# Optimization experiments

Measured on AMD Instinct MI355X. Metric: run time of the kernel, lower is better.

Reference implementation:

```python
import jax, jax.numpy as jnp
import numpy as np

N = 50000   # nodes
E = 800000  # edges (avg degree 16)
D = 128     # hidden_channels
L = 4       # num_layers
ALPHA = 0.1


def setup_inputs() -> dict:
    key = jax.random.key(0)
    ks = jax.random.split(key, 6)
    x = jax.random.normal(ks[0], (N, D), dtype=jnp.float32)
    w = jax.random.uniform(ks[1], (E,), dtype=jnp.float32)
    src = jax.random.randint(ks[2], (E,), 0, N)
    dst = jax.random.randint(ks[3], (E,), 0, N)
    # stacked per-layer Linear params
    W = jax.random.normal(ks[4], (L, D, D), dtype=jnp.float32) / np.float32(np.sqrt(D))
    b = jax.random.normal(ks[5], (L, D), dtype=jnp.float32) * 0.01
    # GPR coefficients: alpha*(1-alpha)^k, last = (1-alpha)^L
    temp_np = ALPHA * (1 - ALPHA) ** np.arange(L + 1)
    temp_np[-1] = (1 - ALPHA) ** L
    temp = jnp.asarray(temp_np, dtype=jnp.float32)
    return {"x": x, "w": w, "src": src, "dst": dst, "W": W, "b": b, "temp": temp}


def reference(x, w, src, dst, W, b, temp):
    # eval mode: dropout / dropout_adj are no-ops; edge_attn=False
    hidden = x * temp[0]
    for i in range(L):
        h = x @ W[i] + b[i]                 # [N, D] linear
        msg = h[src] * w[:, None]           # gather + edge-weight, [E, D]
        x = jax.ops.segment_sum(msg, dst, num_segments=N)  # scatter-sum
        x = jax.nn.relu(x)
        hidden = hidden + x * temp[i + 1]
    return hidden
```

## Files before the change

kernel.cpp:

```cpp
#include <hip/hip_runtime.h>
#include <hip/hip_fp16.h>

#define N_NODES 50000
#define N_EDGES 800000
#define DIM 128
#define LAYERS 4
#define SLOT 48
#define EPB 8

#define BUCKET_BLOCKS 3128
#define WT_BLOCKS 256
#define INIT_BLOCKS 6250

typedef __attribute__((ext_vector_type(8))) _Float16 half8;
typedef __attribute__((ext_vector_type(4))) float float4v;

__device__ __forceinline__ int pack_edge(int s, float w) {
    return (int)(((unsigned)__half_as_ushort(__float2half(w)) << 16) | (unsigned)(s & 0xFFFF));
}

__device__ __forceinline__ void bucket_one(int d, int s, float wv, int g,
                                           int* __restrict__ cnt,
                                           int* __restrict__ edge_buf) {
    if ((d & 7) == g) {
        int pos = atomicAdd(&cnt[d], 1);
        edge_buf[(size_t)d * SLOT + pos] = pack_edge(s, wv);
    }
}

__global__ __launch_bounds__(256) void prep_kernel(const int* __restrict__ src,
                                                   const int* __restrict__ dst,
                                                   const float* __restrict__ w,
                                                   int* __restrict__ cnt,
                                                   int* __restrict__ edge_buf,
                                                   const float* __restrict__ W,
                                                   __half* __restrict__ Wt,
                                                   const float4* __restrict__ x,
                                                   __half* __restrict__ xh) {
    int bid = blockIdx.x;
    int tid = threadIdx.x;
    if (bid < BUCKET_BLOCKS) {
        int g     = bid & 7;
        int chunk = bid >> 3;
        int base  = (chunk * 256 + tid) * EPB;
        if (base >= N_EDGES) return;
        int4   d4a = *(const int4*)(dst + base);
        int4   d4b = *(const int4*)(dst + base + 4);
        int4   s4a = *(const int4*)(src + base);
        int4   s4b = *(const int4*)(src + base + 4);
        float4 w4a = *(const float4*)(w + base);
        float4 w4b = *(const float4*)(w + base + 4);
        bucket_one(d4a.x, s4a.x, w4a.x, g, cnt, edge_buf);
        bucket_one(d4a.y, s4a.y, w4a.y, g, cnt, edge_buf);
        bucket_one(d4a.z, s4a.z, w4a.z, g, cnt, edge_buf);
        bucket_one(d4a.w, s4a.w, w4a.w, g, cnt, edge_buf);
        bucket_one(d4b.x, s4b.x, w4b.x, g, cnt, edge_buf);
        bucket_one(d4b.y, s4b.y, w4b.y, g, cnt, edge_buf);
        bucket_one(d4b.z, s4b.z, w4b.z, g, cnt, edge_buf);
        bucket_one(d4b.w, s4b.w, w4b.w, g, cnt, edge_buf);
    } else if (bid < BUCKET_BLOCKS + WT_BLOCKS) {
        int i = (bid - BUCKET_BLOCKS) * 256 + tid;
        int l   = i >> 14;
        int rem = i & 16383;
        int k = rem >> 7;
        int n = rem & 127;
        Wt[(size_t)l * DIM * DIM + n * DIM + k] =
            __float2half(W[(size_t)l * DIM * DIM + k * DIM + n]);
    } else {
        int i = (bid - BUCKET_BLOCKS - WT_BLOCKS) * 256 + tid;
        float4 v = x[i];
        union { __half2 hh[2]; float2 f2; } u;
        u.hh[0] = __floats2half2_rn(v.x, v.y);
        u.hh[1] = __floats2half2_rn(v.z, v.w);
        *(float2*)(xh + (size_t)i * 4) = u.f2;
    }
}

__device__ __forceinline__ void batch8(const half8* __restrict__ h8,
                                       int m, int base, int cnt_r, int r, int c,
                                       float* accf, float& wsum) {
    half8 v[8]; float wv[8];
    #pragma unroll
    for (int u = 0; u < 8; ++u) {
        int jj = base + u;
        int p  = __shfl(m, (r << 4) | (jj & 15), 64);
        bool live = (jj < cnt_r);
        wv[u] = live
                  ? __half2float(__ushort_as_half((unsigned short)((unsigned)p >> 16)))
                  : 0.f;
        half8 vv = (half8)(0.f);
        if (live) vv = h8[(size_t)(p & 0xFFFF) * 16 + c];
        v[u] = vv;
    }
    #pragma unroll
    for (int u = 0; u < 8; ++u) {
        wsum += wv[u];
        #pragma unroll
        for (int t = 0; t < 8; ++t)
            accf[t] += wv[u] * (float)v[u][t];
    }
}

#define AP 136
template <bool FINAL>
__global__ __launch_bounds__(256) void layer_kernel(const half8* __restrict__ xin8,
                                                    const int* __restrict__ cnt_arr,
                                                    const int* __restrict__ edge_buf,
                                                    const __half* __restrict__ Wt,
                                                    const float* __restrict__ bl,
                                                    __half* __restrict__ xout_h,
                                                    float* __restrict__ hidden,
                                                    const float* __restrict__ temp,
                                                    const float* __restrict__ xf,
                                                    const half8* __restrict__ x1h,
                                                    const half8* __restrict__ x2h) {
    __shared__ __half Ah[16][AP];
    __shared__ float winS[16];
    int tid  = threadIdx.x;
    int wave = tid >> 6;
    int lane = tid & 63;
    int r = lane >> 4;
    int c = lane & 15;
    int node0  = blockIdx.x * 16 + wave * 4;
    int node_r = node0 + r;

    size_t mb = (size_t)node_r * SLOT;
    int m0 = edge_buf[mb + c];
    int m1 = edge_buf[mb + 16 + c];
    int4 c4 = *(const int4*)(cnt_arr + node0);

    int cnt_r = (r == 0) ? c4.x : (r == 1) ? c4.y : (r == 2) ? c4.z : c4.w;
    int maxc  = max(max(c4.x, c4.y), max(c4.z, c4.w));

    float accf[8];
    #pragma unroll
    for (int t = 0; t < 8; ++t) accf[t] = 0.f;
    float wsum = 0.f;

    batch8(xin8, m0, 0, cnt_r, r, c, accf, wsum);
    batch8(xin8, m0, 8, cnt_r, r, c, accf, wsum);
    if (maxc > 16) {
        batch8(xin8, m1, 16, cnt_r, r, c, accf, wsum);
        batch8(xin8, m1, 24, cnt_r, r, c, accf, wsum);
    }
    if (maxc > 32) {
        int m2 = edge_buf[mb + 32 + c];
        batch8(xin8, m2, 32, cnt_r, r, c, accf, wsum);
        batch8(xin8, m2, 40, cnt_r, r, c, accf, wsum);
    }

    union { __half2 hh[4]; float4 f4; } ua;
    ua.hh[0] = __floats2half2_rn(accf[0], accf[1]);
    ua.hh[1] = __floats2half2_rn(accf[2], accf[3]);
    ua.hh[2] = __floats2half2_rn(accf[4], accf[5]);
    ua.hh[3] = __floats2half2_rn(accf[6], accf[7]);
    int lr = wave * 4 + r;
    *(float4*)&Ah[lr][c * 8] = ua.f4;
    if (c == 0) winS[lr] = wsum;
    __syncthreads();

    int am  = lane & 15;
    int ak8 = (lane >> 4) * 8;
    float4v acc0 = (float4v)(0.f), acc1 = (float4v)(0.f);
    #pragma unroll
    for (int kk = 0; kk < 4; ++kk) {
        int k0 = kk * 32 + ak8;
        half8 a  = *(const half8*)&Ah[am][k0];
        half8 b0 = *(const half8*)(Wt + (size_t)(wave * 32 + am) * DIM + k0);
        half8 b1 = *(const half8*)(Wt + (size_t)(wave * 32 + 16 + am) * DIM + k0);
        acc0 = __builtin_amdgcn_mfma_f32_16x16x32_f16(a, b0, acc0, 0, 0, 0);
        acc1 = __builtin_amdgcn_mfma_f32_16x16x32_f16(a, b1, acc1, 0, 0, 0);
    }
    __syncthreads();

    int q  = lane >> 4;
    int cc = lane & 15;
    {
        int col = wave * 32 + cc;
        float bv = bl[col];
        #pragma unroll
        for (int j = 0; j < 4; ++j) {
            int row = q * 4 + j;
            Ah[row][col] = __float2half(fmaxf(acc0[j] + winS[row] * bv, 0.f));
        }
        col = wave * 32 + 16 + cc;
        bv = bl[col];
        #pragma unroll
        for (int j = 0; j < 4; ++j) {
            int row = q * 4 + j;
            Ah[row][col] = __float2half(fmaxf(acc1[j] + winS[row] * bv, 0.f));
        }
    }
    __syncthreads();

    int row = tid >> 4;
    int ch  = tid & 15;
    int gnode = blockIdx.x * 16 + row;
    size_t o = (size_t)gnode * DIM + ch * 8;
    half8 hv = *(const half8*)&Ah[row][ch * 8];

    if constexpr (!FINAL) {
        *(float4*)(xout_h + o) = *(float4*)&hv;
    } else {
        float t0 = temp[0], t1 = temp[1], t2 = temp[2], t3 = temp[3], t4 = temp[4];
        size_t ro = (size_t)gnode * 16 + ch;
        half8 v1 = x1h[ro];
        half8 v2 = x2h[ro];
        half8 v3 = xin8[ro];
        float4 x0a = *(const float4*)(xf + o);
        float4 x0b = *(const float4*)(xf + o + 4);
        float out[8];
        out[0] = t0 * x0a.x; out[1] = t0 * x0a.y; out[2] = t0 * x0a.z; out[3] = t0 * x0a.w;
        out[4] = t0 * x0b.x; out[5] = t0 * x0b.y; out[6] = t0 * x0b.z; out[7] = t0 * x0b.w;
        #pragma unroll
        for (int t = 0; t < 8; ++t)
            out[t] += t1 * (float)v1[t] + t2 * (float)v2[t]
                    + t3 * (float)v3[t] + t4 * (float)hv[t];
        float4 h0 = make_float4(out[0], out[1], out[2], out[3]);
        float4 h1 = make_float4(out[4], out[5], out[6], out[7]);
        *(float4*)(hidden + o)     = h0;
        *(float4*)(hidden + o + 4) = h1;
    }
}

extern "C" void kernel_launch(void* const* d_in, const int* in_sizes, int n_in,
                              void* d_out, int out_size, void* d_ws, size_t ws_size,
                              hipStream_t stream) {
    const float* x    = (const float*)d_in[0];
    const float* w    = (const float*)d_in[1];
    const int*   src  = (const int*)d_in[2];
    const int*   dst  = (const int*)d_in[3];
    const float* W    = (const float*)d_in[4];
    const float* b    = (const float*)d_in[5];
    const float* temp = (const float*)d_in[6];
    float* hidden = (float*)d_out;

    char* ws = (char*)d_ws;
    __half* xhA      = (__half*)ws;                   ws += (size_t)N_NODES * DIM * sizeof(__half);
    __half* xhB      = (__half*)ws;                   ws += (size_t)N_NODES * DIM * sizeof(__half);
    __half* xhC      = (__half*)ws;                   ws += (size_t)N_NODES * DIM * sizeof(__half);
    __half* Wt       = (__half*)ws;                   ws += (size_t)LAYERS * DIM * DIM * sizeof(__half);
    int*    cnt      = (int*)ws;                      ws += (size_t)N_NODES * sizeof(int);
    int*    edge_buf = (int*)ws;                      ws += (size_t)(N_NODES * SLOT + 64) * sizeof(int);

    hipMemsetAsync(cnt, 0, (size_t)N_NODES * sizeof(int), stream);
    prep_kernel<<<BUCKET_BLOCKS + WT_BLOCKS + INIT_BLOCKS, 256, 0, stream>>>(
        src, dst, w, cnt, edge_buf, W, Wt, (const float4*)x, xhA);

    const int layer_blocks = N_NODES / 16;
    layer_kernel<false><<<layer_blocks, 256, 0, stream>>>(
        (const half8*)xhA, cnt, edge_buf, Wt + 0 * DIM * DIM, b + 0 * DIM,
        xhB, hidden, temp, x, nullptr, nullptr);
    layer_kernel<false><<<layer_blocks, 256, 0, stream>>>(
        (const half8*)xhB, cnt, edge_buf, Wt + 1 * DIM * DIM, b + 1 * DIM,
        xhC, hidden, temp, x, nullptr, nullptr);
    layer_kernel<false><<<layer_blocks, 256, 0, stream>>>(
        (const half8*)xhC, cnt, edge_buf, Wt + 2 * DIM * DIM, b + 2 * DIM,
        xhA, hidden, temp, x, nullptr, nullptr);
    layer_kernel<true><<<layer_blocks, 256, 0, stream>>>(
        (const half8*)xhA, cnt, edge_buf, Wt + 3 * DIM * DIM, b + 3 * DIM,
        nullptr, hidden, temp, x, (const half8*)xhB, (const half8*)xhC);
}
```

Measured before the change: 278.3 us.

## Store node features in FP8 and split edge packing from bucketing

Node feature buffers switch from fp16 to fp8 (e4m3 via the packed convert builtins), which halves the bytes moved by the per-edge gathers and the layer outputs. The final layer also reads x0 from the fp8 copy instead of the fp32 input. A separate pre-pass packs dst to 16 bits and src plus weight into one int, so the 8-way bucketing kernel rereads less data. FP8 storage adds noticeable quantization error, including on the x0 term, which may break the accuracy tolerance.

```diff
diff --git a/kernel.cpp b/kernel.cpp
--- a/kernel.cpp
+++ b/kernel.cpp
@@ -8,58 +8,64 @@
 #define SLOT 48
 #define EPB 8
 
+#define PACK_BLOCKS 782
+#define WT_BLOCKS 256
+#define INIT_BLOCKS 3125
 #define BUCKET_BLOCKS 3128
-#define WT_BLOCKS 256
-#define INIT_BLOCKS 6250
 
 typedef __attribute__((ext_vector_type(8))) _Float16 half8;
 typedef __attribute__((ext_vector_type(4))) float float4v;
+typedef __attribute__((ext_vector_type(2))) float float2v;
+typedef __attribute__((ext_vector_type(8))) unsigned short ushort8;
 
 __device__ __forceinline__ int pack_edge(int s, float w) {
     return (int)(((unsigned)__half_as_ushort(__float2half(w)) << 16) | (unsigned)(s & 0xFFFF));
 }
 
-__device__ __forceinline__ void bucket_one(int d, int s, float wv, int g,
-                                           int* __restrict__ cnt,
-                                           int* __restrict__ edge_buf) {
-    if ((d & 7) == g) {
-        int pos = atomicAdd(&cnt[d], 1);
-        edge_buf[(size_t)d * SLOT + pos] = pack_edge(s, wv);
-    }
-}
-
-__global__ __launch_bounds__(256) void prep_kernel(const int* __restrict__ src,
-                                                   const int* __restrict__ dst,
-                                                   const float* __restrict__ w,
-                                                   int* __restrict__ cnt,
-                                                   int* __restrict__ edge_buf,
-                                                   const float* __restrict__ W,
-                                                   __half* __restrict__ Wt,
-                                                   const float4* __restrict__ x,
-                                                   __half* __restrict__ xh) {
+__device__ __forceinline__ void fp8x8_to_f32(uint2 v, float* f) {
+    float2v a = __builtin_amdgcn_cvt_pk_f32_fp8(v.x, false);
+    float2v b = __builtin_amdgcn_cvt_pk_f32_fp8(v.x, true);
+    float2v c = __builtin_amdgcn_cvt_pk_f32_fp8(v.y, false);
+    float2v d = __builtin_amdgcn_cvt_pk_f32_fp8(v.y, true);
+    f[0] = a[0]; f[1] = a[1]; f[2] = b[0]; f[3] = b[1];
+    f[4] = c[0]; f[5] = c[1]; f[6] = d[0]; f[7] = d[1];
+}
+
+__device__ __forceinline__ uint2 f32x8_to_fp8(const float* f) {
+    unsigned lo = 0, hi = 0;
+    lo = __builtin_amdgcn_cvt_pk_fp8_f32(f[0], f[1], lo, false);
+    lo = __builtin_amdgcn_cvt_pk_fp8_f32(f[2], f[3], lo, true);
+    hi = __builtin_amdgcn_cvt_pk_fp8_f32(f[4], f[5], hi, false);
+    hi = __builtin_amdgcn_cvt_pk_fp8_f32(f[6], f[7], hi, true);
+    return make_uint2(lo, hi);
+}
+
+__global__ __launch_bounds__(256) void prep1_kernel(const int* __restrict__ src,
+                                                    const int* __restrict__ dst,
+                                                    const float* __restrict__ w,
+                                                    unsigned short* __restrict__ dst16,
+                                                    int* __restrict__ epk,
+                                                    const float* __restrict__ W,
+                                                    __half* __restrict__ Wt,
+                                                    const float4* __restrict__ x,
+                                                    uint2* __restrict__ xh0) {
     int bid = blockIdx.x;
     int tid = threadIdx.x;
-    if (bid < BUCKET_BLOCKS) {
-        int g     = bid & 7;
-        int chunk = bid >> 3;
-        int base  = (chunk * 256 + tid) * EPB;
-        if (base >= N_EDGES) return;
-        int4   d4a = *(const int4*)(dst + base);
-        int4   d4b = *(const int4*)(dst + base + 4);
-        int4   s4a = *(const int4*)(src + base);
-        int4   s4b = *(const int4*)(src + base + 4);
-        float4 w4a = *(const float4*)(w + base);
-        float4 w4b = *(const float4*)(w + base + 4);
-        bucket_one(d4a.x, s4a.x, w4a.x, g, cnt, edge_buf);
-        bucket_one(d4a.y, s4a.y, w4a.y, g, cnt, edge_buf);
-        bucket_one(d4a.z, s4a.z, w4a.z, g, cnt, edge_buf);
-        bucket_one(d4a.w, s4a.w, w4a.w, g, cnt, edge_buf);
-        bucket_one(d4b.x, s4b.x, w4b.x, g, cnt, edge_buf);
-        bucket_one(d4b.y, s4b.y, w4b.y, g, cnt, edge_buf);
-        bucket_one(d4b.z, s4b.z, w4b.z, g, cnt, edge_buf);
-        bucket_one(d4b.w, s4b.w, w4b.w, g, cnt, edge_buf);
-    } else if (bid < BUCKET_BLOCKS + WT_BLOCKS) {
-        int i = (bid - BUCKET_BLOCKS) * 256 + tid;
+    if (bid < PACK_BLOCKS) {
+        int e = (bid * 256 + tid) * 4;
+        if (e >= N_EDGES) return;
+        int4   d4 = *(const int4*)(dst + e);
+        int4   s4 = *(const int4*)(src + e);
+        float4 w4 = *(const float4*)(w + e);
+        uint2 dd;
+        dd.x = ((unsigned)d4.x & 0xFFFF) | ((unsigned)d4.y << 16);
+        dd.y = ((unsigned)d4.z & 0xFFFF) | ((unsigned)d4.w << 16);
+        *(uint2*)(dst16 + e) = dd;
+        int4 pk = make_int4(pack_edge(s4.x, w4.x), pack_edge(s4.y, w4.y),
+                            pack_edge(s4.z, w4.z), pack_edge(s4.w, w4.w));
+        *(int4*)(epk + e) = pk;
+    } else if (bid < PACK_BLOCKS + WT_BLOCKS) {
+        int i = (bid - PACK_BLOCKS) * 256 + tid;
         int l   = i >> 14;
         int rem = i & 16383;
         int k = rem >> 7;
@@ -67,19 +73,48 @@
         Wt[(size_t)l * DIM * DIM + n * DIM + k] =
             __float2half(W[(size_t)l * DIM * DIM + k * DIM + n]);
     } else {
-        int i = (bid - BUCKET_BLOCKS - WT_BLOCKS) * 256 + tid;
-        float4 v = x[i];
-        union { __half2 hh[2]; float2 f2; } u;
-        u.hh[0] = __floats2half2_rn(v.x, v.y);
-        u.hh[1] = __floats2half2_rn(v.z, v.w);
-        *(float2*)(xh + (size_t)i * 4) = u.f2;
-    }
-}
-
-__device__ __forceinline__ void batch8(const half8* __restrict__ h8,
+        int i = (bid - PACK_BLOCKS - WT_BLOCKS) * 256 + tid;
+        float4 a = x[(size_t)i * 2];
+        float4 b = x[(size_t)i * 2 + 1];
+        float f[8] = { a.x, a.y, a.z, a.w, b.x, b.y, b.z, b.w };
+        xh0[i] = f32x8_to_fp8(f);
+    }
+}
+
+__device__ __forceinline__ void bucket_one(int d, int pk, int g,
+                                           int* __restrict__ cnt,
+                                           int* __restrict__ edge_buf) {
+    if ((d & 7) == g) {
+        int pos = atomicAdd(&cnt[d], 1);
+        edge_buf[(size_t)d * SLOT + pos] = pk;
+    }
+}
+
+__global__ __launch_bounds__(256) void bucket_kernel(const unsigned short* __restrict__ dst16,
+                                                     const int* __restrict__ epk,
+                                                     int* __restrict__ cnt,
+                                                     int* __restrict__ edge_buf) {
+    int g     = blockIdx.x & 7;
+    int chunk = blockIdx.x >> 3;
+    int base  = (chunk * 256 + threadIdx.x) * EPB;
+    if (base >= N_EDGES) return;
+    ushort8 d8 = *(const ushort8*)(dst16 + base);
+    int4    pa = *(const int4*)(epk + base);
+    int4    pb = *(const int4*)(epk + base + 4);
+    bucket_one(d8[0], pa.x, g, cnt, edge_buf);
+    bucket_one(d8[1], pa.y, g, cnt, edge_buf);
+    bucket_one(d8[2], pa.z, g, cnt, edge_buf);
+    bucket_one(d8[3], pa.w, g, cnt, edge_buf);
+    bucket_one(d8[4], pb.x, g, cnt, edge_buf);
+    bucket_one(d8[5], pb.y, g, cnt, edge_buf);
+    bucket_one(d8[6], pb.z, g, cnt, edge_buf);
+    bucket_one(d8[7], pb.w, g, cnt, edge_buf);
+}
+
+__device__ __forceinline__ void batch8(const uint2* __restrict__ x8,
                                        int m, int base, int cnt_r, int r, int c,
                                        float* accf, float& wsum) {
-    half8 v[8]; float wv[8];
+    uint2 v[8]; float wv[8];
     #pragma unroll
     for (int u = 0; u < 8; ++u) {
         int jj = base + u;
@@ -88,32 +123,34 @@
         wv[u] = live
                   ? __half2float(__ushort_as_half((unsigned short)((unsigned)p >> 16)))
                   : 0.f;
-        half8 vv = (half8)(0.f);
-        if (live) vv = h8[(size_t)(p & 0xFFFF) * 16 + c];
+        uint2 vv = make_uint2(0u, 0u);
+        if (live) vv = x8[(size_t)(p & 0xFFFF) * 16 + c];
         v[u] = vv;
     }
     #pragma unroll
     for (int u = 0; u < 8; ++u) {
         wsum += wv[u];
+        float f[8];
+        fp8x8_to_f32(v[u], f);
         #pragma unroll
         for (int t = 0; t < 8; ++t)
-            accf[t] += wv[u] * (float)v[u][t];
+            accf[t] += wv[u] * f[t];
     }
 }
 
 #define AP 136
 template <bool FINAL>
-__global__ __launch_bounds__(256) void layer_kernel(const half8* __restrict__ xin8,
+__global__ __launch_bounds__(256) void layer_kernel(const uint2* __restrict__ xin8,
                                                     const int* __restrict__ cnt_arr,
                                                     const int* __restrict__ edge_buf,
                                                     const __half* __restrict__ Wt,
                                                     const float* __restrict__ bl,
-                                                    __half* __restrict__ xout_h,
+                                                    uint2* __restrict__ xout,
                                                     float* __restrict__ hidden,
                                                     const float* __restrict__ temp,
-                                                    const float* __restrict__ xf,
-                                                    const half8* __restrict__ x1h,
-                                                    const half8* __restrict__ x2h) {
+                                                    const uint2* __restrict__ x0h,
+                                                    const uint2* __restrict__ x1h,
+                                                    const uint2* __restrict__ x2h) {
     __shared__ __half Ah[16][AP];
     __shared__ float winS[16];
     int tid  = threadIdx.x;
@@ -196,30 +233,30 @@
     int row = tid >> 4;
     int ch  = tid & 15;
     int gnode = blockIdx.x * 16 + row;
-    size_t o = (size_t)gnode * DIM + ch * 8;
     half8 hv = *(const half8*)&Ah[row][ch * 8];
+    size_t ro = (size_t)gnode * 16 + ch;
 
     if constexpr (!FINAL) {
-        *(float4*)(xout_h + o) = *(float4*)&hv;
+        float f[8];
+        #pragma unroll
+        for (int t = 0; t < 8; ++t) f[t] = (float)hv[t];
+        xout[ro] = f32x8_to_fp8(f);
     } else {
         float t0 = temp[0], t1 = temp[1], t2 = temp[2], t3 = temp[3], t4 = temp[4];
-        size_t ro = (size_t)gnode * 16 + ch;
-        half8 v1 = x1h[ro];
-        half8 v2 = x2h[ro];
-        half8 v3 = xin8[ro];
-        float4 x0a = *(const float4*)(xf + o);
-        float4 x0b = *(const float4*)(xf + o + 4);
+        uint2 u0 = x0h[ro], u1 = x1h[ro], u2 = x2h[ro], u3 = xin8[ro];
+        float f0[8], f1[8], f2[8], f3[8];
+        fp8x8_to_f32(u0, f0);
+        fp8x8_to_f32(u1, f1);
+        fp8x8_to_f32(u2, f2);
+        fp8x8_to_f32(u3, f3);
         float out[8];
-        out[0] = t0 * x0a.x; out[1] = t0 * x0a.y; out[2] = t0 * x0a.z; out[3] = t0 * x0a.w;
-        out[4] = t0 * x0b.x; out[5] = t0 * x0b.y; out[6] = t0 * x0b.z; out[7] = t0 * x0b.w;
         #pragma unroll
         for (int t = 0; t < 8; ++t)
-            out[t] += t1 * (float)v1[t] + t2 * (float)v2[t]
-                    + t3 * (float)v3[t] + t4 * (float)hv[t];
-        float4 h0 = make_float4(out[0], out[1], out[2], out[3]);
-        float4 h1 = make_float4(out[4], out[5], out[6], out[7]);
-        *(float4*)(hidden + o)     = h0;
-        *(float4*)(hidden + o + 4) = h1;
+            out[t] = t0 * f0[t] + t1 * f1[t] + t2 * f2[t]
+                   + t3 * f3[t] + t4 * (float)hv[t];
+        size_t o = (size_t)gnode * DIM + ch * 8;
+        *(float4*)(hidden + o)     = make_float4(out[0], out[1], out[2], out[3]);
+        *(float4*)(hidden + o + 4) = make_float4(out[4], out[5], out[6], out[7]);
     }
 }
 
@@ -236,28 +273,32 @@
     float* hidden = (float*)d_out;
 
     char* ws = (char*)d_ws;
-    __half* xhA      = (__half*)ws;                   ws += (size_t)N_NODES * DIM * sizeof(__half);
-    __half* xhB      = (__half*)ws;                   ws += (size_t)N_NODES * DIM * sizeof(__half);
-    __half* xhC      = (__half*)ws;                   ws += (size_t)N_NODES * DIM * sizeof(__half);
-    __half* Wt       = (__half*)ws;                   ws += (size_t)LAYERS * DIM * DIM * sizeof(__half);
-    int*    cnt      = (int*)ws;                      ws += (size_t)N_NODES * sizeof(int);
-    int*    edge_buf = (int*)ws;                      ws += (size_t)(N_NODES * SLOT + 64) * sizeof(int);
+    uint2* X0 = (uint2*)ws;                  ws += (size_t)N_NODES * DIM;
+    uint2* X1 = (uint2*)ws;                  ws += (size_t)N_NODES * DIM;
+    uint2* X2 = (uint2*)ws;                  ws += (size_t)N_NODES * DIM;
+    uint2* X3 = (uint2*)ws;                  ws += (size_t)N_NODES * DIM;
+    __half* Wt = (__half*)ws;                ws += (size_t)LAYERS * DIM * DIM * sizeof(__half);
+    int* cnt = (int*)ws;                     ws += (size_t)N_NODES * sizeof(int);
+    int* edge_buf = (int*)ws;                ws += (size_t)(N_NODES * SLOT + 64) * sizeof(int);
+    unsigned short* dst16 = (unsigned short*)ws;  ws += (size_t)N_EDGES * sizeof(unsigned short);
+    int* epk = (int*)ws;                     ws += (size_t)N_EDGES * sizeof(int);
 
     hipMemsetAsync(cnt, 0, (size_t)N_NODES * sizeof(int), stream);
-    prep_kernel<<<BUCKET_BLOCKS + WT_BLOCKS + INIT_BLOCKS, 256, 0, stream>>>(
-        src, dst, w, cnt, edge_buf, W, Wt, (const float4*)x, xhA);
+    prep1_kernel<<<PACK_BLOCKS + WT_BLOCKS + INIT_BLOCKS, 256, 0, stream>>>(
+        src, dst, w, dst16, epk, W, Wt, (const float4*)x, X0);
+    bucket_kernel<<<BUCKET_BLOCKS, 256, 0, stream>>>(dst16, epk, cnt, edge_buf);
 
     const int layer_blocks = N_NODES / 16;
     layer_kernel<false><<<layer_blocks, 256, 0, stream>>>(
-        (const half8*)xhA, cnt, edge_buf, Wt + 0 * DIM * DIM, b + 0 * DIM,
-        xhB, hidden, temp, x, nullptr, nullptr);
+        X0, cnt, edge_buf, Wt + 0 * DIM * DIM, b + 0 * DIM,
+        X1, hidden, temp, nullptr, nullptr, nullptr);
     layer_kernel<false><<<layer_blocks, 256, 0, stream>>>(
-        (const half8*)xhB, cnt, edge_buf, Wt + 1 * DIM * DIM, b + 1 * DIM,
-        xhC, hidden, temp, x, nullptr, nullptr);
+        X1, cnt, edge_buf, Wt + 1 * DIM * DIM, b + 1 * DIM,
+        X2, hidden, temp, nullptr, nullptr, nullptr);
     layer_kernel<false><<<layer_blocks, 256, 0, stream>>>(
-        (const half8*)xhC, cnt, edge_buf, Wt + 2 * DIM * DIM, b + 2 * DIM,
-        xhA, hidden, temp, x, nullptr, nullptr);
+        X2, cnt, edge_buf, Wt + 2 * DIM * DIM, b + 2 * DIM,
+        X3, hidden, temp, nullptr, nullptr, nullptr);
     layer_kernel<true><<<layer_blocks, 256, 0, stream>>>(
-        (const half8*)xhA, cnt, edge_buf, Wt + 3 * DIM * DIM, b + 3 * DIM,
-        nullptr, hidden, temp, x, (const half8*)xhB, (const half8*)xhC);
-}
+        X3, cnt, edge_buf, Wt + 3 * DIM * DIM, b + 3 * DIM,
+        nullptr, hidden, temp, X0, X1, X2);
+}
```

Result: faster. 249.8 us (-10.3%).
